# Kernel optimization log

Hardware: AMD Instinct MI355X
Metric: run time of the kernel (lower is better)

The kernel has to match this reference:

```python
import jax, jax.numpy as jnp
import numpy as np

N = 100000   # nodes
E = 1600000  # edges
D_IN = 128
H = 64
L = 3        # num SAGE layers
G = 512      # graphs in batch


def setup_inputs() -> dict:
    key = jax.random.key(0)
    ks = jax.random.split(key, 12)
    s = 0.05
    return {
        "x": jax.random.normal(ks[0], (N, D_IN), dtype=jnp.float32),
        "edge_index": jax.random.randint(ks[1], (2, E), 0, N, dtype=jnp.int64),
        "edge_attr": jax.random.normal(ks[2], (E, 1), dtype=jnp.float32),
        "batch": jnp.sort(jax.random.randint(ks[3], (N,), 0, G, dtype=jnp.int64)),
        "W0": jax.random.normal(ks[4], (D_IN, H), dtype=jnp.float32) * s,
        "b0": jnp.zeros((H,), dtype=jnp.float32),
        "Wl": jax.random.normal(ks[5], (L, H, H), dtype=jnp.float32) * s,  # lin_l (aggregated neighbors), has bias
        "bl": jnp.zeros((L, H), dtype=jnp.float32),
        "Wr": jax.random.normal(ks[6], (L, H, H), dtype=jnp.float32) * s,  # lin_r (root), no bias
        "W1": jax.random.normal(ks[7], (H, H), dtype=jnp.float32) * s,
        "b1": jnp.zeros((H,), dtype=jnp.float32),
    }


def reference(x, edge_index, edge_attr, batch, W0, b0, Wl, bl, Wr, W1, b1):
    # edge_attr is accepted but unused, matching the torch module.
    h = jax.nn.relu(x @ W0 + b0)                    # [N, H]
    src, dst = edge_index[0], edge_index[1]
    ones_e = jnp.ones((E,), dtype=h.dtype)
    deg = jax.ops.segment_sum(ones_e, dst, num_segments=N)
    deg = jnp.clip(deg, 1.0)[:, None]               # avoid div by zero (PyG mean -> 0 for isolated)
    for i in range(L):
        # SAGEConv: mean-aggregate source features onto targets, then lin_l(agg)+lin_r(h)
        agg = jax.ops.segment_sum(h[src], dst, num_segments=N) / deg  # [N, H]
        h = jax.nn.relu(agg @ Wl[i] + bl[i] + h @ Wr[i])
    # global_mean_pool over batch ids
    cnt = jax.ops.segment_sum(jnp.ones((N,), dtype=h.dtype), batch, num_segments=G)
    pooled = jax.ops.segment_sum(h, batch, num_segments=G) / jnp.clip(cnt, 1.0)[:, None]  # [G, H]
    return pooled @ W1 + b1                          # [G, H]
```

## Files before the change

### kernel.cpp

```cpp
#include <hip/hip_runtime.h>
#include <hip/hip_bf16.h>

#define NN 100000
#define NE 1600000
#define DIN 128
#define NG 512
#define MAXD 64
#define NBUK 391
#define BCAP 5120
#define CHUNK ((NE + NBUK - 1) / NBUK)
#define NTILE ((NN + 63) >> 6)

typedef __attribute__((ext_vector_type(8))) __bf16 bf16x8;
typedef __attribute__((ext_vector_type(4))) float f32x4;

static __device__ __forceinline__ unsigned short bfhi(float f) {
    __hip_bfloat16 h = __float2bfloat16(f);
    return *reinterpret_cast<unsigned short*>(&h);
}
static __device__ __forceinline__ float bf2f(unsigned short u) {
    unsigned v = (unsigned)u << 16;
    return __uint_as_float(v);
}
static __device__ __forceinline__ bf16x8 ldfrag(const void* p) {
    bf16x8 r;
    __builtin_memcpy(&r, p, 16);
    return r;
}
static __device__ __forceinline__ int swz(int a) {
    return a ^ (((a >> 8) & 3) << 5) ^ (((a >> 12) & 3) << 4);
}


#define GB 256
__global__ void __launch_bounds__(512) k_front(const int* __restrict__ src,
                                               const int* __restrict__ dst,
                                               int* __restrict__ cursor,
                                               unsigned int* __restrict__ bucket,
                                               const float* __restrict__ x,
                                               const float* __restrict__ W0,
                                               const float* __restrict__ b0,
                                               float* __restrict__ h) {
    __shared__ unsigned short sS[2 * 8192];
    __shared__ int lcnt[NBUK];
    __shared__ int lbase[NBUK];
    if (blockIdx.x < NBUK) {
        for (int i = threadIdx.x; i < NBUK; i += 512) lcnt[i] = 0;
        __syncthreads();
        int e0 = blockIdx.x * CHUNK;
        int e1 = min(e0 + CHUNK, NE);
        for (int e = e0 + (int)threadIdx.x; e < e1; e += 512)
            atomicAdd(&lcnt[dst[e] >> 8], 1);
        __syncthreads();
        for (int i = threadIdx.x; i < NBUK; i += 512) {
            int c = lcnt[i];
            lbase[i] = c ? atomicAdd(&cursor[i], c) : 0;
            lcnt[i] = 0;
        }
        __syncthreads();
        for (int e = e0 + (int)threadIdx.x; e < e1; e += 512) {
            int d = dst[e];
            int s = src[e];
            int bk = d >> 8;
            int pos = lbase[bk] + atomicAdd(&lcnt[bk], 1);
            if (pos < BCAP)
                bucket[(size_t)bk * BCAP + pos] = ((unsigned)s << 8) | (unsigned)(d & 255);
        }
    } else {
        unsigned short* sP0 = sS;
        unsigned short* sP1 = sS + 8192;
        for (int i = threadIdx.x; i < 8192; i += 512) {
            int k = i >> 6, c = i & 63;
            int slot = ((k >> 5) << 2) | (c >> 4);
            int ln   = (((k >> 3) & 3) << 4) | (c & 15);
            int ba   = swz((((((slot << 6) | ln) << 3) | (k & 7)) << 1));
            float w0 = W0[i];
            unsigned short hh = bfhi(w0);
            *(unsigned short*)((char*)sP0 + ba) = hh;
            *(unsigned short*)((char*)sP1 + ba) = bfhi(w0 - bf2f(hh));
        }
        __syncthreads();
        int lane = threadIdx.x & 63;
        int wv   = threadIdx.x >> 6;
        int cb   = wv & 3;
        int rbh  = wv >> 2;
        int col  = (cb << 4) | (lane & 15);
        float bj = b0[col];
        int r0   = (lane >> 4) << 2;
        bf16x8 Bh[4], Bl[4];
#pragma unroll
        for (int ks = 0; ks < 4; ++ks) {
            int bb = swz(((((ks << 2) | cb) << 6) | lane) << 4);
            Bh[ks] = ldfrag((const char*)sP0 + bb);
            Bl[ks] = ldfrag((const char*)sP1 + bb);
        }
        for (int t = blockIdx.x - NBUK; t < NTILE; t += GB) {
            int n0 = t << 6;
            __syncthreads();
#pragma unroll
            for (int i = 0; i < 4; ++i) {
                int tau = (int)threadIdx.x + (i << 9);
                int r = tau >> 5, kq = tau & 31;
                int n = n0 + r;
                float4 v = make_float4(0.f, 0.f, 0.f, 0.f);
                if (n < NN) v = *(const float4*)(x + ((size_t)n << 7) + (kq << 2));
                int k0   = kq << 2;
                int slot = ((k0 >> 5) << 2) | (r >> 4);
                int ln   = (((k0 >> 3) & 3) << 4) | (r & 15);
                int ba   = swz((((((slot << 6) | ln) << 3) | (k0 & 7)) << 1));
                unsigned short h0 = bfhi(v.x), h1 = bfhi(v.y),
                               h2 = bfhi(v.z), h3 = bfhi(v.w);
                *(ushort4*)((char*)sP0 + ba) = make_ushort4(h0, h1, h2, h3);
                *(ushort4*)((char*)sP1 + ba) = make_ushort4(
                    bfhi(v.x - bf2f(h0)), bfhi(v.y - bf2f(h1)),
                    bfhi(v.z - bf2f(h2)), bfhi(v.w - bf2f(h3)));
            }
            __syncthreads();
            f32x4 acc[2] = {{0.f,0.f,0.f,0.f},{0.f,0.f,0.f,0.f}};
#pragma unroll
            for (int ks = 0; ks < 4; ++ks) {
#pragma unroll
                for (int rl = 0; rl < 2; ++rl) {
                    int rb = (rbh << 1) | rl;
                    int ab = swz(((((ks << 2) | rb) << 6) | lane) << 4);
                    bf16x8 ah = ldfrag((const char*)sP0 + ab);
                    bf16x8 al = ldfrag((const char*)sP1 + ab);
                    acc[rl] = __builtin_amdgcn_mfma_f32_16x16x32_bf16(ah, Bh[ks], acc[rl], 0, 0, 0);
                    acc[rl] = __builtin_amdgcn_mfma_f32_16x16x32_bf16(ah, Bl[ks], acc[rl], 0, 0, 0);
                    acc[rl] = __builtin_amdgcn_mfma_f32_16x16x32_bf16(al, Bh[ks], acc[rl], 0, 0, 0);
                }
            }
#pragma unroll
            for (int rl = 0; rl < 2; ++rl) {
                int rb = (rbh << 1) | rl;
#pragma unroll
                for (int reg = 0; reg < 4; ++reg) {
                    int row = (rb << 4) + r0 + reg;
                    int n = n0 + row;
                    if (n < NN)
                        h[((size_t)n << 6) + col] = fmaxf(acc[rl][reg] + bj, 0.f);
                }
            }
        }
    }
}

__device__ __forceinline__ void gemmLR_mfma(unsigned short* sS,
                                            int tid, int nblk, int bidx,
                                            float* __restrict__ h_r,
                                            __hip_bfloat16* __restrict__ g,
                                            const float* __restrict__ Wl,
                                            const float* __restrict__ bl,
                                            const float* __restrict__ Wr) {
    unsigned short* sP0 = sS;
    unsigned short* sP1 = sS + 4096;
    int lane = tid & 63;
    int cb   = tid >> 6;
    bf16x8 BLh[2], BLl[2], BRh[2], BRl[2];
    for (int i = tid; i < 4096; i += 256) {
        int k = i >> 6, c = i & 63;
        int slot = ((k >> 5) << 2) | (c >> 4);
        int ln   = (((k >> 3) & 3) << 4) | (c & 15);
        int ba   = swz((((((slot << 6) | ln) << 3) | (k & 7)) << 1));
        float w = Wl[i];
        unsigned short hh = bfhi(w);
        *(unsigned short*)((char*)sP0 + ba) = hh;
        *(unsigned short*)((char*)sP1 + ba) = bfhi(w - bf2f(hh));
    }
    __syncthreads();
#pragma unroll
    for (int ks = 0; ks < 2; ++ks) {
        int bb = swz(((((ks << 2) | cb) << 6) | lane) << 4);
        BLh[ks] = ldfrag((const char*)sP0 + bb);
        BLl[ks] = ldfrag((const char*)sP1 + bb);
    }
    __syncthreads();
    for (int i = tid; i < 4096; i += 256) {
        int k = i >> 6, c = i & 63;
        int slot = ((k >> 5) << 2) | (c >> 4);
        int ln   = (((k >> 3) & 3) << 4) | (c & 15);
        int ba   = swz((((((slot << 6) | ln) << 3) | (k & 7)) << 1));
        float w = Wr[i];
        unsigned short hh = bfhi(w);
        *(unsigned short*)((char*)sP0 + ba) = hh;
        *(unsigned short*)((char*)sP1 + ba) = bfhi(w - bf2f(hh));
    }
    __syncthreads();
#pragma unroll
    for (int ks = 0; ks < 2; ++ks) {
        int bb = swz(((((ks << 2) | cb) << 6) | lane) << 4);
        BRh[ks] = ldfrag((const char*)sP0 + bb);
        BRl[ks] = ldfrag((const char*)sP1 + bb);
    }
    int col = (cb << 4) | (lane & 15);
    float bj = bl[col];
    int r0  = (lane >> 4) << 2;
    unsigned short* gp = (unsigned short*)g;
    for (int t = bidx; t < NTILE; t += nblk) {
        int n0 = t << 6;
        __syncthreads();
#pragma unroll
        for (int i = 0; i < 4; ++i) {
            int tau = tid + (i << 8);
            int r = tau >> 4, kq = tau & 15;
            int n = n0 + r;
            float4 v = make_float4(0.f, 0.f, 0.f, 0.f);
            if (n < NN) v = *(const float4*)(h_r + ((size_t)n << 6) + (kq << 2));
            int k0   = kq << 2;
            int slot = ((k0 >> 5) << 2) | (r >> 4);
            int ln   = (((k0 >> 3) & 3) << 4) | (r & 15);
            int ba   = swz((((((slot << 6) | ln) << 3) | (k0 & 7)) << 1));
            unsigned short h0 = bfhi(v.x), h1 = bfhi(v.y),
                           h2 = bfhi(v.z), h3 = bfhi(v.w);
            *(ushort4*)((char*)sP0 + ba) = make_ushort4(h0, h1, h2, h3);
            *(ushort4*)((char*)sP1 + ba) = make_ushort4(
                bfhi(v.x - bf2f(h0)), bfhi(v.y - bf2f(h1)),
                bfhi(v.z - bf2f(h2)), bfhi(v.w - bf2f(h3)));
        }
        __syncthreads();
        f32x4 accl[4] = {{0.f,0.f,0.f,0.f},{0.f,0.f,0.f,0.f},
                         {0.f,0.f,0.f,0.f},{0.f,0.f,0.f,0.f}};
        f32x4 accr[4] = {{0.f,0.f,0.f,0.f},{0.f,0.f,0.f,0.f},
                         {0.f,0.f,0.f,0.f},{0.f,0.f,0.f,0.f}};
#pragma unroll
        for (int ks = 0; ks < 2; ++ks) {
#pragma unroll
            for (int rb = 0; rb < 4; ++rb) {
                int ab = swz(((((ks << 2) | rb) << 6) | lane) << 4);
                bf16x8 ah = ldfrag((const char*)sP0 + ab);
                bf16x8 al = ldfrag((const char*)sP1 + ab);
                accl[rb] = __builtin_amdgcn_mfma_f32_16x16x32_bf16(ah, BLh[ks], accl[rb], 0, 0, 0);
                accl[rb] = __builtin_amdgcn_mfma_f32_16x16x32_bf16(ah, BLl[ks], accl[rb], 0, 0, 0);
                accl[rb] = __builtin_amdgcn_mfma_f32_16x16x32_bf16(al, BLh[ks], accl[rb], 0, 0, 0);
                accr[rb] = __builtin_amdgcn_mfma_f32_16x16x32_bf16(ah, BRh[ks], accr[rb], 0, 0, 0);
                accr[rb] = __builtin_amdgcn_mfma_f32_16x16x32_bf16(ah, BRl[ks], accr[rb], 0, 0, 0);
                accr[rb] = __builtin_amdgcn_mfma_f32_16x16x32_bf16(al, BRh[ks], accr[rb], 0, 0, 0);
            }
        }
#pragma unroll
        for (int rb = 0; rb < 4; ++rb) {
#pragma unroll
            for (int reg = 0; reg < 4; ++reg) {
                int row = (rb << 4) + r0 + reg;
                int n = n0 + row;
                if (n < NN) {
                    size_t o = ((size_t)n << 6) + col;
                    gp[o]  = bfhi(accl[rb][reg]);
                    h_r[o] = accr[rb][reg] + bj;
                }
            }
        }
    }
}

#define MGB 512
__global__ void __launch_bounds__(256) k_mid(const unsigned int* __restrict__ bucket,
                                             const int* __restrict__ cursor,
                                             int* __restrict__ cnt,
                                             int* __restrict__ ell,
                                             float* __restrict__ h_r,
                                             __hip_bfloat16* __restrict__ g,
                                             const float* __restrict__ Wl,
                                             const float* __restrict__ bl,
                                             const float* __restrict__ Wr) {
    __shared__ unsigned short sS[2 * 4096];
    __shared__ int lc[256];
    if (blockIdx.x < NBUK) {
        lc[threadIdx.x] = 0;
        int b = blockIdx.x;
        __syncthreads();
        int m = min(cursor[b], BCAP);
        const unsigned int* bp = bucket + (size_t)b * BCAP;
        for (int i = threadIdx.x; i < m; i += 256) {
            unsigned v = bp[i];
            int dlo = (int)(v & 255u);
            int s   = (int)(v >> 8);
            int p   = atomicAdd(&lc[dlo], 1);
            if (p < MAXD)
                ell[(((size_t)b << 8) + dlo) * MAXD + p] = s;
        }
        __syncthreads();
        int n = (b << 8) + (int)threadIdx.x;
        if (n < NN) cnt[n] = lc[threadIdx.x];
    } else {
        gemmLR_mfma(sS, threadIdx.x, MGB, blockIdx.x - NBUK, h_r, g, Wl, bl, Wr);
    }
}

#define ACCU(U) { \
    a0 += __uint_as_float((U).x << 16); a1 += __uint_as_float((U).x & 0xffff0000u); \
    a2 += __uint_as_float((U).y << 16); a3 += __uint_as_float((U).y & 0xffff0000u); \
    a4 += __uint_as_float((U).z << 16); a5 += __uint_as_float((U).z & 0xffff0000u); \
    a6 += __uint_as_float((U).w << 16); a7 += __uint_as_float((U).w & 0xffff0000u); }

#define FB 512
__global__ void __launch_bounds__(512) k_gg(const uint4* __restrict__ gin,
                                            float* __restrict__ rA,
                                            unsigned short* __restrict__ gout,
                                            const int* __restrict__ cnt,
                                            const int* __restrict__ ell,
                                            const float* __restrict__ Wl,
                                            const float* __restrict__ bl,
                                            const float* __restrict__ Wr) {
    __shared__ unsigned short sS[2 * 4096];
    unsigned short* sP0 = sS;
    unsigned short* sP1 = sS + 4096;
    int tid = (int)threadIdx.x;
    int lane = tid & 63;
    int w    = tid >> 6;
    int cb   = w & 3;
    int rbh  = w >> 2;
    bf16x8 BLh[2], BLl[2], BRh[2], BRl[2];
    for (int i = tid; i < 4096; i += 512) {
        int k = i >> 6, c = i & 63;
        int slot = ((k >> 5) << 2) | (c >> 4);
        int ln   = (((k >> 3) & 3) << 4) | (c & 15);
        int ba   = swz((((((slot << 6) | ln) << 3) | (k & 7)) << 1));
        float wv_ = Wl[i];
        unsigned short hh = bfhi(wv_);
        *(unsigned short*)((char*)sP0 + ba) = hh;
        *(unsigned short*)((char*)sP1 + ba) = bfhi(wv_ - bf2f(hh));
    }
    __syncthreads();
#pragma unroll
    for (int ks = 0; ks < 2; ++ks) {
        int bb = swz(((((ks << 2) | cb) << 6) | lane) << 4);
        BLh[ks] = ldfrag((const char*)sP0 + bb);
        BLl[ks] = ldfrag((const char*)sP1 + bb);
    }
    __syncthreads();
    for (int i = tid; i < 4096; i += 512) {
        int k = i >> 6, c = i & 63;
        int slot = ((k >> 5) << 2) | (c >> 4);
        int ln   = (((k >> 3) & 3) << 4) | (c & 15);
        int ba   = swz((((((slot << 6) | ln) << 3) | (k & 7)) << 1));
        float wv_ = Wr[i];
        unsigned short hh = bfhi(wv_);
        *(unsigned short*)((char*)sP0 + ba) = hh;
        *(unsigned short*)((char*)sP1 + ba) = bfhi(wv_ - bf2f(hh));
    }
    __syncthreads();
#pragma unroll
    for (int ks = 0; ks < 2; ++ks) {
        int bb = swz(((((ks << 2) | cb) << 6) | lane) << 4);
        BRh[ks] = ldfrag((const char*)sP0 + bb);
        BRl[ks] = ldfrag((const char*)sP1 + bb);
    }
    int col = (cb << 4) | (lane & 15);
    float bj = bl[col];
    int r0  = (lane >> 4) << 2;
    int o   = lane >> 3;
    int c8  = lane & 7;
    for (int t = blockIdx.x; t < NTILE; t += FB) {
        int n0t = t << 6;
        int myn = n0t + (w << 3) + o;
        int d = (myn < NN) ? cnt[myn] : 0;
        int dc = min(d, MAXD);
        int dm = max(dc, __shfl_xor(dc, 8));
        dm     = max(dm, __shfl_xor(dm, 16));
        dm     = max(dm, __shfl_xor(dm, 32));
        int iters = (dm + 7) & ~7;
        const int* er = ell + ((size_t)min(myn, NN - 1) << 6) + (c8 << 3);
        int4 l0 = *(const int4*)er;
        int4 l1 = *(const int4*)(er + 4);
        float a0=0.f,a1=0.f,a2=0.f,a3=0.f,a4=0.f,a5=0.f,a6=0.f,a7=0.f;
        for (int j0 = 0; j0 < iters; j0 += 8) {
            int sl = (o << 3) | (j0 >> 3);
            int i0 = __shfl(l0.x, sl);
            int i1 = __shfl(l0.y, sl);
            int i2 = __shfl(l0.z, sl);
            int i3 = __shfl(l0.w, sl);
            int i4 = __shfl(l1.x, sl);
            int i5 = __shfl(l1.y, sl);
            int i6 = __shfl(l1.z, sl);
            int i7 = __shfl(l1.w, sl);
            i0 = (j0 + 0 < d) ? i0 : NN;
            i1 = (j0 + 1 < d) ? i1 : NN;
            i2 = (j0 + 2 < d) ? i2 : NN;
            i3 = (j0 + 3 < d) ? i3 : NN;
            i4 = (j0 + 4 < d) ? i4 : NN;
            i5 = (j0 + 5 < d) ? i5 : NN;
            i6 = (j0 + 6 < d) ? i6 : NN;
            i7 = (j0 + 7 < d) ? i7 : NN;
            uint4 u0 = gin[(size_t)i0 * 8 + c8];
            uint4 u1 = gin[(size_t)i1 * 8 + c8];
            uint4 u2 = gin[(size_t)i2 * 8 + c8];
            uint4 u3 = gin[(size_t)i3 * 8 + c8];
            uint4 u4 = gin[(size_t)i4 * 8 + c8];
            uint4 u5 = gin[(size_t)i5 * 8 + c8];
            uint4 u6 = gin[(size_t)i6 * 8 + c8];
            uint4 u7 = gin[(size_t)i7 * 8 + c8];
            ACCU(u0); ACCU(u1); ACCU(u2); ACCU(u3);
            ACCU(u4); ACCU(u5); ACCU(u6); ACCU(u7);
        }
        float4 rv0 = make_float4(0.f,0.f,0.f,0.f), rv1 = rv0;
        if (myn < NN) {
            float inv = 1.0f / fmaxf((float)d, 1.0f);
            const float4* rp = (const float4*)(rA + ((size_t)myn << 6) + (c8 << 3));
            rv0 = rp[0]; rv1 = rp[1];
            rv0.x = fmaxf(fmaf(a0, inv, rv0.x), 0.0f);
            rv0.y = fmaxf(fmaf(a1, inv, rv0.y), 0.0f);
            rv0.z = fmaxf(fmaf(a2, inv, rv0.z), 0.0f);
            rv0.w = fmaxf(fmaf(a3, inv, rv0.w), 0.0f);
            rv1.x = fmaxf(fmaf(a4, inv, rv1.x), 0.0f);
            rv1.y = fmaxf(fmaf(a5, inv, rv1.y), 0.0f);
            rv1.z = fmaxf(fmaf(a6, inv, rv1.z), 0.0f);
            rv1.w = fmaxf(fmaf(a7, inv, rv1.w), 0.0f);
        }
        __syncthreads();
        {
            int rr = (w << 3) + o;
#pragma unroll
            for (int half = 0; half < 2; ++half) {
                float4 v = half ? rv1 : rv0;
                int k0 = (c8 << 3) + (half << 2);
                int slot = ((k0 >> 5) << 2) | (rr >> 4);
                int ln   = (((k0 >> 3) & 3) << 4) | (rr & 15);
                int ba   = swz((((((slot << 6) | ln) << 3) | (k0 & 7)) << 1));
                unsigned short h0 = bfhi(v.x), h1 = bfhi(v.y),
                               h2 = bfhi(v.z), h3 = bfhi(v.w);
                *(ushort4*)((char*)sP0 + ba) = make_ushort4(h0, h1, h2, h3);
                *(ushort4*)((char*)sP1 + ba) = make_ushort4(
                    bfhi(v.x - bf2f(h0)), bfhi(v.y - bf2f(h1)),
                    bfhi(v.z - bf2f(h2)), bfhi(v.w - bf2f(h3)));
            }
        }
        __syncthreads();
        f32x4 accl[2] = {{0.f,0.f,0.f,0.f},{0.f,0.f,0.f,0.f}};
        f32x4 accr[2] = {{0.f,0.f,0.f,0.f},{0.f,0.f,0.f,0.f}};
#pragma unroll
        for (int ks = 0; ks < 2; ++ks) {
#pragma unroll
            for (int rl = 0; rl < 2; ++rl) {
                int rb = (rbh << 1) | rl;
                int ab = swz(((((ks << 2) | rb) << 6) | lane) << 4);
                bf16x8 ah = ldfrag((const char*)sP0 + ab);
                bf16x8 al = ldfrag((const char*)sP1 + ab);
                accl[rl] = __builtin_amdgcn_mfma_f32_16x16x32_bf16(ah, BLh[ks], accl[rl], 0, 0, 0);
                accl[rl] = __builtin_amdgcn_mfma_f32_16x16x32_bf16(ah, BLl[ks], accl[rl], 0, 0, 0);
                accl[rl] = __builtin_amdgcn_mfma_f32_16x16x32_bf16(al, BLh[ks], accl[rl], 0, 0, 0);
                accr[rl] = __builtin_amdgcn_mfma_f32_16x16x32_bf16(ah, BRh[ks], accr[rl], 0, 0, 0);
                accr[rl] = __builtin_amdgcn_mfma_f32_16x16x32_bf16(ah, BRl[ks], accr[rl], 0, 0, 0);
                accr[rl] = __builtin_amdgcn_mfma_f32_16x16x32_bf16(al, BRh[ks], accr[rl], 0, 0, 0);
            }
        }
#pragma unroll
        for (int rl = 0; rl < 2; ++rl) {
            int rb = (rbh << 1) | rl;
#pragma unroll
            for (int reg = 0; reg < 4; ++reg) {
                int row = (rb << 4) + r0 + reg;
                int n = n0t + row;
                if (n < NN) {
                    size_t off = ((size_t)n << 6) + col;
                    gout[off] = bfhi(accl[rl][reg]);
                    rA[off]   = accr[rl][reg] + bj;
                }
            }
        }
    }
}

__global__ void __launch_bounds__(256) k_gather(const uint4* __restrict__ g4,
                                                float* __restrict__ r_h,
                                                const int* __restrict__ cnt,
                                                const int* __restrict__ ell) {
    int lane = threadIdx.x & 63;
    int o    = lane >> 3;
    int c8   = lane & 7;
    int wv = __builtin_amdgcn_readfirstlane((int)((blockIdx.x * 256 + threadIdx.x) >> 6));
    int nw = (gridDim.x * 256) >> 6;
    for (int p = wv; p < NN / 8; p += nw) {
        int myn = 8 * p + o;
        int d   = cnt[myn];
        int dc  = min(d, MAXD);
        int dm  = max(dc, __shfl_xor(dc, 8));
        dm      = max(dm, __shfl_xor(dm, 16));
        dm      = max(dm, __shfl_xor(dm, 32));
        int iters = (dm + 7) & ~7;
        const int* er = ell + ((size_t)myn << 6) + (c8 << 3);
        int4 l0 = *(const int4*)er;
        int4 l1 = *(const int4*)(er + 4);
        float a0=0.f,a1=0.f,a2=0.f,a3=0.f,a4=0.f,a5=0.f,a6=0.f,a7=0.f;
        for (int j0 = 0; j0 < iters; j0 += 8) {
            int sl = (o << 3) | (j0 >> 3);
            int i0 = __shfl(l0.x, sl);
            int i1 = __shfl(l0.y, sl);
            int i2 = __shfl(l0.z, sl);
            int i3 = __shfl(l0.w, sl);
            int i4 = __shfl(l1.x, sl);
            int i5 = __shfl(l1.y, sl);
            int i6 = __shfl(l1.z, sl);
            int i7 = __shfl(l1.w, sl);
            i0 = (j0 + 0 < d) ? i0 : NN;
            i1 = (j0 + 1 < d) ? i1 : NN;
            i2 = (j0 + 2 < d) ? i2 : NN;
            i3 = (j0 + 3 < d) ? i3 : NN;
            i4 = (j0 + 4 < d) ? i4 : NN;
            i5 = (j0 + 5 < d) ? i5 : NN;
            i6 = (j0 + 6 < d) ? i6 : NN;
            i7 = (j0 + 7 < d) ? i7 : NN;
            uint4 u0 = g4[(size_t)i0 * 8 + c8];
            uint4 u1 = g4[(size_t)i1 * 8 + c8];
            uint4 u2 = g4[(size_t)i2 * 8 + c8];
            uint4 u3 = g4[(size_t)i3 * 8 + c8];
            uint4 u4 = g4[(size_t)i4 * 8 + c8];
            uint4 u5 = g4[(size_t)i5 * 8 + c8];
            uint4 u6 = g4[(size_t)i6 * 8 + c8];
            uint4 u7 = g4[(size_t)i7 * 8 + c8];
            ACCU(u0); ACCU(u1); ACCU(u2); ACCU(u3);
            ACCU(u4); ACCU(u5); ACCU(u6); ACCU(u7);
        }
        float inv = 1.0f / fmaxf((float)d, 1.0f);
        float4* rp = (float4*)(r_h + ((size_t)myn << 6) + (c8 << 3));
        float4 rv0 = rp[0], rv1 = rp[1];
        rv0.x = fmaxf(fmaf(a0, inv, rv0.x), 0.0f);
        rv0.y = fmaxf(fmaf(a1, inv, rv0.y), 0.0f);
        rv0.z = fmaxf(fmaf(a2, inv, rv0.z), 0.0f);
        rv0.w = fmaxf(fmaf(a3, inv, rv0.w), 0.0f);
        rv1.x = fmaxf(fmaf(a4, inv, rv1.x), 0.0f);
        rv1.y = fmaxf(fmaf(a5, inv, rv1.y), 0.0f);
        rv1.z = fmaxf(fmaf(a6, inv, rv1.z), 0.0f);
        rv1.w = fmaxf(fmaf(a7, inv, rv1.w), 0.0f);
        rp[0] = rv0; rp[1] = rv1;
    }
}

__global__ void __launch_bounds__(256) k_pool(const int* __restrict__ batch,
                                              const float* __restrict__ h,
                                              float* __restrict__ pool,
                                              float* __restrict__ cntg) {
    int lane = threadIdx.x & 63;
    int wid  = (blockIdx.x * 256 + threadIdx.x) >> 6;
    int nw   = (gridDim.x * 256) >> 6;
    int chunk = (NN + nw - 1) / nw;
    int n0 = wid * chunk;
    if (n0 >= NN) return;
    int n1 = min(n0 + chunk, NN);
    int cur = batch[n0];
    float acc = 0.0f, acc_c = 0.0f;
    for (int n = n0; n < n1; ++n) {
        int b = batch[n];
        if (b != cur) {
            atomicAdd(&pool[(size_t)cur * 64 + lane], acc);
            if (lane == 0) atomicAdd(&cntg[cur], acc_c);
            acc = 0.0f; acc_c = 0.0f; cur = b;
        }
        acc   += h[(size_t)n * 64 + lane];
        acc_c += 1.0f;
    }
    atomicAdd(&pool[(size_t)cur * 64 + lane], acc);
    if (lane == 0) atomicAdd(&cntg[cur], acc_c);
}

__global__ void __launch_bounds__(256) k_out(const float* __restrict__ pool,
                                             const float* __restrict__ cntg,
                                             const float* __restrict__ W1,
                                             const float* __restrict__ b1,
                                             float* __restrict__ out) {
    __shared__ float sW[64 * 64];
    for (int i = threadIdx.x; i < 64 * 64; i += 256) sW[i] = W1[i];
    __syncthreads();
    int lane = threadIdx.x & 63;
    int wid  = (blockIdx.x * 256 + threadIdx.x) >> 6;
    int nw   = (gridDim.x * 256) >> 6;
    for (int gidx = wid; gidx < NG; gidx += nw) {
        float ic = 1.0f / fmaxf(cntg[gidx], 1.0f);
        float acc = 0.0f;
#pragma unroll
        for (int k = 0; k < 64; ++k)
            acc = fmaf(pool[(size_t)gidx * 64 + k], sW[k * 64 + lane], acc);
        out[(size_t)gidx * 64 + lane] = fmaf(acc, ic, b1[lane]);
    }
}

extern "C" void kernel_launch(void* const* d_in, const int* in_sizes, int n_in,
                              void* d_out, int out_size, void* d_ws, size_t ws_size,
                              hipStream_t stream) {
    const float* x     = (const float*)d_in[0];
    const int*   ei    = (const int*)d_in[1];
    const int*   batch = (const int*)d_in[3];
    const float* W0    = (const float*)d_in[4];
    const float* b0    = (const float*)d_in[5];
    const float* Wl    = (const float*)d_in[6];
    const float* bl    = (const float*)d_in[7];
    const float* Wr    = (const float*)d_in[8];
    const float* W1    = (const float*)d_in[9];
    const float* b1    = (const float*)d_in[10];
    float* out = (float*)d_out;

    char* ws = (char*)d_ws;
    size_t off = 0;
    auto alloc = [&](size_t bytes) -> void* {
        void* p = ws + off;
        off += (bytes + 255) & ~(size_t)255;
        return p;
    };
    float*          A  = (float*)alloc((size_t)NN * 64 * 4);
    unsigned short* G0 = (unsigned short*)alloc((size_t)NN * 128);
    size_t z1start = off;
    (void)alloc(256);
    unsigned short* G1 = (unsigned short*)alloc((size_t)NN * 128);
    size_t z2start = off;
    (void)alloc(256);
    int*   cursor = (int*)alloc((size_t)NBUK * 4);
    float* pool   = (float*)alloc((size_t)NG * 64 * 4);
    float* cntg   = (float*)alloc((size_t)NG * 4);
    size_t z2len = off - z2start;
    int*          ell    = (int*)alloc((size_t)NN * MAXD * 4);
    unsigned int* bucket = (unsigned int*)alloc((size_t)NBUK * BCAP * 4);
    int*          cnt    = (int*)alloc((size_t)NN * 4);

    const int* src = ei;
    const int* dst = ei + NE;

    hipMemsetAsync(ws + z1start, 0, 256, stream);
    hipMemsetAsync(ws + z2start, 0, z2len, stream);

    k_front<<<NBUK + GB, 512, 0, stream>>>(src, dst, cursor, bucket, x, W0, b0, A);
    k_mid<<<NBUK + MGB, 256, 0, stream>>>(bucket, cursor, cnt, ell, A,
                                          (__hip_bfloat16*)G0, Wl, bl, Wr);
    k_gg<<<FB, 512, 0, stream>>>((const uint4*)G0, A, G1, cnt, ell,
                                 Wl + (size_t)1 * 64 * 64, bl + 64, Wr + (size_t)1 * 64 * 64);
    k_gg<<<FB, 512, 0, stream>>>((const uint4*)G1, A, G0, cnt, ell,
                                 Wl + (size_t)2 * 64 * 64, bl + 128, Wr + (size_t)2 * 64 * 64);
    k_gather<<<3125, 256, 0, stream>>>((const uint4*)G0, A, cnt, ell);

    k_pool<<<256, 256, 0, stream>>>(batch, A, pool, cntg);
    k_out<<<128, 256, 0, stream>>>(pool, cntg, W1, b1, out);
}
```

Before: 377.7 us.

## Fuse final gather with mean pooling and enlarge grid sizes

The last neighbor-gather kernel now computes the final ReLU activations and accumulates them straight into the per-graph pool buffer. It reduces across the 8 nodes in a wavefront with shuffles when they share a graph, and falls back to per-node atomics otherwise. This removes the write-back of the final hidden state, the re-read by a separate pooling kernel, and one launch, at the cost of more global float atomics. Grid sizes for the front, mid and per-layer GEMM/gather kernels are also raised to expose more parallelism.

```diff
diff --git a/kernel.cpp b/kernel.cpp
--- a/kernel.cpp
+++ b/kernel.cpp
@@ -32,7 +32,7 @@
 }
 
 
-#define GB 256
+#define GB 512
 __global__ void __launch_bounds__(512) k_front(const int* __restrict__ src,
                                                const int* __restrict__ dst,
                                                int* __restrict__ cursor,
@@ -253,7 +253,7 @@
     }
 }
 
-#define MGB 512
+#define MGB 1024
 __global__ void __launch_bounds__(256) k_mid(const unsigned int* __restrict__ bucket,
                                              const int* __restrict__ cursor,
                                              int* __restrict__ cnt,
@@ -293,7 +293,7 @@
     a4 += __uint_as_float((U).z << 16); a5 += __uint_as_float((U).z & 0xffff0000u); \
     a6 += __uint_as_float((U).w << 16); a7 += __uint_as_float((U).w & 0xffff0000u); }
 
-#define FB 512
+#define FB 1568
 __global__ void __launch_bounds__(512) k_gg(const uint4* __restrict__ gin,
                                             float* __restrict__ rA,
                                             unsigned short* __restrict__ gout,
@@ -461,10 +461,13 @@
     }
 }
 
-__global__ void __launch_bounds__(256) k_gather(const uint4* __restrict__ g4,
-                                                float* __restrict__ r_h,
-                                                const int* __restrict__ cnt,
-                                                const int* __restrict__ ell) {
+__global__ void __launch_bounds__(256) k_gpool(const uint4* __restrict__ g4,
+                                               const float* __restrict__ rA,
+                                               const int* __restrict__ cnt,
+                                               const int* __restrict__ ell,
+                                               const int* __restrict__ batch,
+                                               float* __restrict__ pool,
+                                               float* __restrict__ cntg) {
     int lane = threadIdx.x & 63;
     int o    = lane >> 3;
     int c8   = lane & 7;
@@ -512,45 +515,43 @@
             ACCU(u4); ACCU(u5); ACCU(u6); ACCU(u7);
         }
         float inv = 1.0f / fmaxf((float)d, 1.0f);
-        float4* rp = (float4*)(r_h + ((size_t)myn << 6) + (c8 << 3));
+        const float4* rp = (const float4*)(rA + ((size_t)myn << 6) + (c8 << 3));
         float4 rv0 = rp[0], rv1 = rp[1];
-        rv0.x = fmaxf(fmaf(a0, inv, rv0.x), 0.0f);
-        rv0.y = fmaxf(fmaf(a1, inv, rv0.y), 0.0f);
-        rv0.z = fmaxf(fmaf(a2, inv, rv0.z), 0.0f);
-        rv0.w = fmaxf(fmaf(a3, inv, rv0.w), 0.0f);
-        rv1.x = fmaxf(fmaf(a4, inv, rv1.x), 0.0f);
-        rv1.y = fmaxf(fmaf(a5, inv, rv1.y), 0.0f);
-        rv1.z = fmaxf(fmaf(a6, inv, rv1.z), 0.0f);
-        rv1.w = fmaxf(fmaf(a7, inv, rv1.w), 0.0f);
-        rp[0] = rv0; rp[1] = rv1;
-    }
-}
-
-__global__ void __launch_bounds__(256) k_pool(const int* __restrict__ batch,
-                                              const float* __restrict__ h,
-                                              float* __restrict__ pool,
-                                              float* __restrict__ cntg) {
-    int lane = threadIdx.x & 63;
-    int wid  = (blockIdx.x * 256 + threadIdx.x) >> 6;
-    int nw   = (gridDim.x * 256) >> 6;
-    int chunk = (NN + nw - 1) / nw;
-    int n0 = wid * chunk;
-    if (n0 >= NN) return;
-    int n1 = min(n0 + chunk, NN);
-    int cur = batch[n0];
-    float acc = 0.0f, acc_c = 0.0f;
-    for (int n = n0; n < n1; ++n) {
-        int b = batch[n];
-        if (b != cur) {
-            atomicAdd(&pool[(size_t)cur * 64 + lane], acc);
-            if (lane == 0) atomicAdd(&cntg[cur], acc_c);
-            acc = 0.0f; acc_c = 0.0f; cur = b;
-        }
-        acc   += h[(size_t)n * 64 + lane];
-        acc_c += 1.0f;
-    }
-    atomicAdd(&pool[(size_t)cur * 64 + lane], acc);
-    if (lane == 0) atomicAdd(&cntg[cur], acc_c);
+        float v0 = fmaxf(fmaf(a0, inv, rv0.x), 0.0f);
+        float v1 = fmaxf(fmaf(a1, inv, rv0.y), 0.0f);
+        float v2 = fmaxf(fmaf(a2, inv, rv0.z), 0.0f);
+        float v3 = fmaxf(fmaf(a3, inv, rv0.w), 0.0f);
+        float v4 = fmaxf(fmaf(a4, inv, rv1.x), 0.0f);
+        float v5 = fmaxf(fmaf(a5, inv, rv1.y), 0.0f);
+        float v6 = fmaxf(fmaf(a6, inv, rv1.z), 0.0f);
+        float v7 = fmaxf(fmaf(a7, inv, rv1.w), 0.0f);
+        int b  = batch[myn];
+        int b0 = __shfl(b, c8);
+        if (__all(b == b0)) {
+#pragma unroll
+            for (int m = 8; m <= 32; m <<= 1) {
+                v0 += __shfl_xor(v0, m); v1 += __shfl_xor(v1, m);
+                v2 += __shfl_xor(v2, m); v3 += __shfl_xor(v3, m);
+                v4 += __shfl_xor(v4, m); v5 += __shfl_xor(v5, m);
+                v6 += __shfl_xor(v6, m); v7 += __shfl_xor(v7, m);
+            }
+            if (o == 0) {
+                float* pb = pool + ((size_t)b0 << 6) + (c8 << 3);
+                atomicAdd(pb + 0, v0); atomicAdd(pb + 1, v1);
+                atomicAdd(pb + 2, v2); atomicAdd(pb + 3, v3);
+                atomicAdd(pb + 4, v4); atomicAdd(pb + 5, v5);
+                atomicAdd(pb + 6, v6); atomicAdd(pb + 7, v7);
+                if (c8 == 0) atomicAdd(&cntg[b0], 8.0f);
+            }
+        } else {
+            float* pb = pool + ((size_t)b << 6) + (c8 << 3);
+            atomicAdd(pb + 0, v0); atomicAdd(pb + 1, v1);
+            atomicAdd(pb + 2, v2); atomicAdd(pb + 3, v3);
+            atomicAdd(pb + 4, v4); atomicAdd(pb + 5, v5);
+            atomicAdd(pb + 6, v6); atomicAdd(pb + 7, v7);
+            if (c8 == 0) atomicAdd(&cntg[b], 1.0f);
+        }
+    }
 }
 
 __global__ void __launch_bounds__(256) k_out(const float* __restrict__ pool,
@@ -624,8 +625,7 @@
                                  Wl + (size_t)1 * 64 * 64, bl + 64, Wr + (size_t)1 * 64 * 64);
     k_gg<<<FB, 512, 0, stream>>>((const uint4*)G1, A, G0, cnt, ell,
                                  Wl + (size_t)2 * 64 * 64, bl + 128, Wr + (size_t)2 * 64 * 64);
-    k_gather<<<3125, 256, 0, stream>>>((const uint4*)G0, A, cnt, ell);
-
-    k_pool<<<256, 256, 0, stream>>>(batch, A, pool, cntg);
+    k_gpool<<<3125, 256, 0, stream>>>((const uint4*)G0, A, cnt, ell, batch, pool, cntg);
+
     k_out<<<128, 256, 0, stream>>>(pool, cntg, W1, b1, out);
 }
```

After: 432.6 us. 1.15x slower.
